# Optimization experiments

Measured on AMD Instinct MI355X. Metric: run time of the kernel, lower is better.

Reference implementation:

```python
import jax, jax.numpy as jnp
import numpy as np

B, CIN, H, W = 1, 512, 128, 128
NC, D, P, NH = 10, 128, 200, 8
HW = H * W
DH = D // NH
FF = 256


def setup_inputs():
    key = jax.random.key(0)
    ks = jax.random.split(key, 20)
    def nrm(i, shape, s=0.02):
        return jax.random.normal(ks[i], shape, jnp.float32) * s
    # TransFusion create_2D_grid: pixel-center coords (x, y), flattened to [1, HW, 2]
    xs = jnp.arange(W, dtype=jnp.float32) + 0.5
    ys = jnp.arange(H, dtype=jnp.float32) + 0.5
    gx, gy = jnp.meshgrid(xs, ys, indexing='xy')
    bev_pos = jnp.stack([gx.reshape(-1), gy.reshape(-1)], axis=-1)[None]
    return {
        'x': jax.random.normal(ks[0], (B, CIN, H, W), jnp.float32),
        'w_shared': nrm(1, (D, CIN, 3, 3)), 'b_shared': jnp.zeros((D,), jnp.float32),
        'w_heat': nrm(2, (NC, D, 3, 3)), 'b_heat': jnp.full((NC,), -2.19, jnp.float32),
        'classes_eye': jnp.eye(NC, dtype=jnp.float32),
        'bev_pos': bev_pos,
        'w_ce': nrm(3, (D, NC)), 'b_ce': jnp.zeros((D,), jnp.float32),
        'w_qpos': nrm(4, (D, 2)), 'w_kpos': nrm(5, (D, 2)),
        'wq': nrm(6, (D, D)), 'wk': nrm(7, (D, D)), 'wv': nrm(8, (D, D)), 'wo': nrm(9, (D, D)),
        'ln1_g': jnp.ones((D,), jnp.float32), 'ln1_b': jnp.zeros((D,), jnp.float32),
        'ln2_g': jnp.ones((D,), jnp.float32), 'ln2_b': jnp.zeros((D,), jnp.float32),
        'w_ff1': nrm(10, (FF, D)), 'b_ff1': jnp.zeros((FF,), jnp.float32),
        'w_ff2': nrm(11, (D, FF)), 'b_ff2': jnp.zeros((D,), jnp.float32),
        'w_center': nrm(12, (2, D)), 'b_center': jnp.zeros((2,), jnp.float32),
        'w_height': nrm(13, (1, D)), 'b_height': jnp.zeros((1,), jnp.float32),
        'w_dim': nrm(14, (3, D)), 'b_dim': jnp.zeros((3,), jnp.float32),
        'w_rot': nrm(15, (2, D)), 'b_rot': jnp.zeros((2,), jnp.float32),
        'w_vel': nrm(16, (2, D)), 'b_vel': jnp.zeros((2,), jnp.float32),
        'w_hm': nrm(17, (NC, D)), 'b_hm': jnp.zeros((NC,), jnp.float32),
    }


def _conv2d(x, w, b):
    y = jax.lax.conv_general_dilated(x, w, (1, 1), 'SAME',
                                     dimension_numbers=('NCHW', 'OIHW', 'NCHW'))
    return y + b[None, :, None, None]


def _ln(x, g, b):
    m = jnp.mean(x, -1, keepdims=True)
    v = jnp.var(x, -1, keepdims=True)
    return (x - m) * jax.lax.rsqrt(v + 1e-5) * g + b


def reference(x, w_shared, b_shared, w_heat, b_heat, classes_eye, bev_pos,
              w_ce, b_ce, w_qpos, w_kpos, wq, wk, wv, wo,
              ln1_g, ln1_b, ln2_g, ln2_b, w_ff1, b_ff1, w_ff2, b_ff2,
              w_center, b_center, w_height, b_height, w_dim, b_dim,
              w_rot, b_rot, w_vel, b_vel, w_hm, b_hm):
    lidar_feat = jax.nn.relu(_conv2d(x, w_shared, b_shared))          # [B,D,H,W]
    lidar_flat = lidar_feat.reshape(B, D, HW)
    dense_heatmap = _conv2d(lidar_feat, w_heat, b_heat)               # [B,NC,H,W]
    heatmap = jax.lax.stop_gradient(jax.nn.sigmoid(dense_heatmap))    # .detach().sigmoid()
    # 3x3 local-max 'NMS'; zero-initialized border (F.max_pool2d VALID placed into zeros)
    inner = jax.lax.reduce_window(heatmap, -jnp.inf, jax.lax.max,
                                  (1, 1, 3, 3), (1, 1, 1, 1), 'VALID')
    local_max = jnp.zeros_like(heatmap).at[:, :, 1:-1, 1:-1].set(inner)
    local_max = local_max.at[:, 8].set(heatmap[:, 8])  # nuScenes: no NMS for cls 8,9
    local_max = local_max.at[:, 9].set(heatmap[:, 9])
    heatmap = heatmap * (heatmap == local_max)
    hm_flat = heatmap.reshape(B, NC, HW)
    # top-k proposals over flattened class*position axis
    _, top = jax.lax.top_k(hm_flat.reshape(B, -1), P)
    top_cls = top // HW                                               # [B,P]
    top_idx = top % HW                                                # [B,P]
    query_feat = jnp.take_along_axis(
        lidar_flat, jnp.broadcast_to(top_idx[:, None, :], (B, D, P)), axis=2)
    one_hot = classes_eye[top_cls].transpose(0, 2, 1)                 # [B,NC,P]
    # class encoding: 1x1 conv1d on one-hot
    query_feat = query_feat + jnp.einsum('dc,bcp->bdp', w_ce, one_hot) + b_ce[None, :, None]
    query_pos = jnp.take_along_axis(
        jnp.broadcast_to(bev_pos, (B, HW, 2)),
        jnp.broadcast_to(top_idx[:, :, None], (B, P, 2)), axis=1)     # [B,P,2]
    # single decoder layer: cross-attention of proposals over BEV features
    q_in = query_feat.transpose(0, 2, 1) + query_pos @ w_qpos.T       # [B,P,D]
    kv_in = lidar_flat.transpose(0, 2, 1) + bev_pos @ w_kpos.T        # [B,HW,D]
    q = (q_in @ wq.T).reshape(B, P, NH, DH)
    k = (kv_in @ wk.T).reshape(B, HW, NH, DH)
    v = (kv_in @ wv.T).reshape(B, HW, NH, DH)
    attn = jax.nn.softmax(jnp.einsum('bqhd,bkhd->bhqk', q, k) / np.sqrt(DH).astype(np.float32), axis=-1)
    out = jnp.einsum('bhqk,bkhd->bqhd', attn, v).reshape(B, P, D) @ wo.T
    h1 = _ln(query_feat.transpose(0, 2, 1) + out, ln1_g, ln1_b)
    ff = jax.nn.relu(h1 @ w_ff1.T + b_ff1) @ w_ff2.T + b_ff2
    h2 = _ln(h1 + ff, ln2_g, ln2_b)
    feat = h2.transpose(0, 2, 1)                                      # [B,D,P]
    def head(wt, bt):
        return jnp.einsum('od,bdp->bop', wt, feat) + bt[None, :, None]
    center = head(w_center, b_center) + query_pos.transpose(0, 2, 1)
    height = head(w_height, b_height)
    dim = head(w_dim, b_dim)
    rot = head(w_rot, b_rot)
    vel = head(w_vel, b_vel)
    hm_pred = head(w_hm, b_hm)
    query_heatmap_score = jnp.take_along_axis(
        hm_flat, jnp.broadcast_to(top_idx[:, None, :], (B, NC, P)), axis=2)
    # get_bboxes: sigmoid(heatmap) * query_heatmap_score * one_hot
    score = jax.nn.sigmoid(hm_pred) * query_heatmap_score * one_hot
    return (score, rot, dim, center, height, vel)
```

## Files before the change

kernel.cpp:

```cpp
#include <hip/hip_runtime.h>
#include <math.h>

#define HWSZ 16384

typedef __attribute__((ext_vector_type(8))) short short8;
typedef __attribute__((ext_vector_type(8))) unsigned short ush8;
typedef __attribute__((ext_vector_type(4))) float f4;

__device__ __forceinline__ ushort f2bf(float f) {
    unsigned u = __float_as_uint(f);
    return (ushort)((u + 0x7fffu + ((u >> 16) & 1u)) >> 16);
}
__device__ __forceinline__ float bf2f(ushort b) {
    return __uint_as_float(((unsigned)b) << 16);
}

__global__ void k_prep_w2(const float* __restrict__ w, float* __restrict__ wt) {
    int idx = blockIdx.x * 256 + threadIdx.x;
    if (idx >= 1152 * 16) return;
    int k = idx >> 4, oc = idx & 15;
    wt[idx] = (oc < 10) ? w[oc * 1152 + k] : 0.f;
}
__global__ void k_cvt_w(const float* __restrict__ w, ushort* __restrict__ wh,
                        ushort* __restrict__ wl) {
    int idx = blockIdx.x * 256 + threadIdx.x;
    if (idx >= 589824) return;
    int oc = idx / 4608, r = idx - oc * 4608;
    int tap = r >> 9, c = r & 511;
    float f = w[oc * 4608 + c * 9 + tap];
    ushort hb = f2bf(f);
    wh[idx] = hb;
    wl[idx] = f2bf(f - bf2f(hb));
}
__global__ __launch_bounds__(256) void k_cvt_x(const float* __restrict__ x,
        ushort* __restrict__ xh, ushort* __restrict__ xl) {
    __shared__ float T[64 * 65];
    int hw0 = blockIdx.x << 6;
    int c0 = blockIdx.y << 6;
    int t = threadIdx.x;
    {
        int cl = t >> 2, q = t & 3;
        const float* src = x + (size_t)(c0 + cl) * HWSZ + hw0 + q * 16;
        #pragma unroll
        for (int k = 0; k < 4; k++) {
            float4 v = *reinterpret_cast<const float4*>(src + k * 4);
            float* dst = &T[cl * 65 + q * 16 + k * 4];
            dst[0] = v.x; dst[1] = v.y; dst[2] = v.z; dst[3] = v.w;
        }
    }
    __syncthreads();
    {
        int hwl = t >> 2, q = t & 3;
        int cc = q * 16;
        size_t ob = (size_t)(hw0 + hwl) * 512 + c0 + cc;
        #pragma unroll
        for (int half = 0; half < 2; half++) {
            ush8 hv, lv;
            #pragma unroll
            for (int k = 0; k < 8; k++) {
                float f = T[(cc + half * 8 + k) * 65 + hwl];
                ushort hb = f2bf(f);
                hv[k] = hb;
                lv[k] = f2bf(f - bf2f(hb));
            }
            *reinterpret_cast<ush8*>(xh + ob + half * 8) = hv;
            *reinterpret_cast<ush8*>(xl + ob + half * 8) = lv;
        }
    }
}

__global__ __launch_bounds__(256) void k_conv1_mfma(
        const ushort* __restrict__ xh, const ushort* __restrict__ xl,
        const ushort* __restrict__ wh, const ushort* __restrict__ wl,
        const float* __restrict__ bias, float* __restrict__ out) {
    __shared__ ushort smem[30720];
    const int t = threadIdx.x;
    const int h = blockIdx.x >> 1, w0 = (blockIdx.x & 1) << 6;
    const int l = t & 63;
    const int wid = t >> 6;
    const int wm = wid >> 1, wn = wid & 1;
    const int l15 = l & 15, lhi = l >> 4;
    const int arow = t >> 2, achk = t & 3;

    f4 acc[2][4];
    #pragma unroll
    for (int m = 0; m < 2; m++)
        #pragma unroll
        for (int n = 0; n < 4; n++) acc[m][n] = (f4){0.f, 0.f, 0.f, 0.f};

    short8 rA[2], rB[2][2];
    const short8 zz = {0, 0, 0, 0, 0, 0, 0, 0};

    auto issue = [&](int it) {
        int c0 = (it / 9) << 5;
        int tap = it % 9;
        int dh = tap / 3 - 1, dw = tap % 3 - 1;
        int hh = h + dh;
        int wg = w0 + arow + dw;
        if (hh >= 0 && hh < 128 && wg >= 0 && wg < 128) {
            size_t off = ((size_t)(hh * 128 + wg) << 9) + c0 + (achk << 3);
            rA[0] = *reinterpret_cast<const short8*>(xh + off);
            rA[1] = *reinterpret_cast<const short8*>(xl + off);
        } else { rA[0] = zz; rA[1] = zz; }
        #pragma unroll
        for (int u = 0; u < 2; u++) {
            int oc = (u << 6) + (t >> 2);
            size_t off = (size_t)oc * 4608 + tap * 512 + c0 + (achk << 3);
            rB[u][0] = *reinterpret_cast<const short8*>(wh + off);
            rB[u][1] = *reinterpret_cast<const short8*>(wl + off);
        }
    };
    auto wstage = [&](int buf) {
        *reinterpret_cast<short8*>(&smem[buf * 5120 + arow * 40 + achk * 8]) = rA[0];
        *reinterpret_cast<short8*>(&smem[buf * 5120 + 2560 + arow * 40 + achk * 8]) = rA[1];
        #pragma unroll
        for (int u = 0; u < 2; u++) {
            int oc = (u << 6) + (t >> 2);
            *reinterpret_cast<short8*>(&smem[10240 + buf * 10240 + oc * 40 + achk * 8]) = rB[u][0];
            *reinterpret_cast<short8*>(&smem[10240 + buf * 10240 + 5120 + oc * 40 + achk * 8]) = rB[u][1];
        }
    };

    issue(0);
    wstage(0);
    issue(1);
    __syncthreads();

    for (int it = 0; it < 144; ++it) {
        int buf = it & 1;
        short8 aH[2], aL[2], bH[4], bL[4];
        #pragma unroll
        for (int m = 0; m < 2; m++) {
            int row = wm * 32 + m * 16 + l15;
            aH[m] = *reinterpret_cast<const short8*>(&smem[buf * 5120 + row * 40 + lhi * 8]);
            aL[m] = *reinterpret_cast<const short8*>(&smem[buf * 5120 + 2560 + row * 40 + lhi * 8]);
        }
        #pragma unroll
        for (int n = 0; n < 4; n++) {
            int oc = wn * 64 + n * 16 + l15;
            bH[n] = *reinterpret_cast<const short8*>(&smem[10240 + buf * 10240 + oc * 40 + lhi * 8]);
            bL[n] = *reinterpret_cast<const short8*>(&smem[10240 + buf * 10240 + 5120 + oc * 40 + lhi * 8]);
        }
        #pragma unroll
        for (int m = 0; m < 2; m++)
            #pragma unroll
            for (int n = 0; n < 4; n++) {
                acc[m][n] = __builtin_amdgcn_mfma_f32_16x16x32_bf16(aH[m], bH[n], acc[m][n], 0, 0, 0);
                acc[m][n] = __builtin_amdgcn_mfma_f32_16x16x32_bf16(aL[m], bH[n], acc[m][n], 0, 0, 0);
                acc[m][n] = __builtin_amdgcn_mfma_f32_16x16x32_bf16(aH[m], bL[n], acc[m][n], 0, 0, 0);
            }
        if (it + 1 < 144) {
            wstage(buf ^ 1);
            if (it + 2 < 144) issue(it + 2);
        }
        __syncthreads();
    }

    float* ot = reinterpret_cast<float*>(smem);
    #pragma unroll
    for (int m = 0; m < 2; m++)
        #pragma unroll
        for (int n = 0; n < 4; n++) {
            int oc = wn * 64 + n * 16 + l15;
            float b = bias[oc];
            #pragma unroll
            for (int r = 0; r < 4; r++) {
                int px = wm * 32 + m * 16 + lhi * 4 + r;
                ot[px * 132 + oc] = fmaxf(acc[m][n][r] + b, 0.f);
            }
        }
    __syncthreads();
    {
        int oc = t >> 1, half = t & 1;
        int base = h * 128 + w0 + half * 32;
        #pragma unroll
        for (int i = 0; i < 32; i += 4) {
            float4 v;
            v.x = ot[(half * 32 + i + 0) * 132 + oc];
            v.y = ot[(half * 32 + i + 1) * 132 + oc];
            v.z = ot[(half * 32 + i + 2) * 132 + oc];
            v.w = ot[(half * 32 + i + 3) * 132 + oc];
            *reinterpret_cast<float4*>(&out[(size_t)oc * HWSZ + base + i]) = v;
        }
    }
}

__global__ __launch_bounds__(256) void k_conv2(const float* __restrict__ lidar,
        const float* __restrict__ wt, const float* __restrict__ bias,
        float* __restrict__ sig) {
    __shared__ float xs[16 * 3 * 68];
    __shared__ float wsm[144 * 16];
    int bid = blockIdx.x;
    int h = bid >> 1, w0 = (bid & 1) << 6;
    int t = threadIdx.x;
    int tpx = (t & 15) << 2;
    int oc = t >> 4;
    float acc[4] = {0.f, 0.f, 0.f, 0.f};
    for (int c0 = 0; c0 < 128; c0 += 16) {
        for (int i = t; i < 16 * 3 * 66; i += 256) {
            int c = i / 198; int rem = i - c * 198; int r = rem / 66; int j = rem - r * 66;
            int gr = h - 1 + r, gc = w0 - 1 + j;
            float v = 0.f;
            if (((unsigned)gr < 128u) & ((unsigned)gc < 128u))
                v = lidar[(c0 + c) * HWSZ + gr * 128 + gc];
            xs[(c * 3 + r) * 68 + j] = v;
        }
        {
            const float4* src = (const float4*)(wt + c0 * 9 * 16);
            float4* dst = (float4*)wsm;
            for (int i = t; i < 576; i += 256) dst[i] = src[i];
        }
        __syncthreads();
        #pragma unroll 4
        for (int c = 0; c < 16; c++) {
            #pragma unroll
            for (int kh = 0; kh < 3; kh++) {
                const float* xr = &xs[(c * 3 + kh) * 68 + tpx];
                float xv0 = xr[0], xv1 = xr[1], xv2 = xr[2], xv3 = xr[3], xv4 = xr[4], xv5 = xr[5];
                #pragma unroll
                for (int kw = 0; kw < 3; kw++) {
                    float wv = wsm[(c * 9 + kh * 3 + kw) * 16 + oc];
                    float p0 = (kw == 0) ? xv0 : ((kw == 1) ? xv1 : xv2);
                    float p1 = (kw == 0) ? xv1 : ((kw == 1) ? xv2 : xv3);
                    float p2 = (kw == 0) ? xv2 : ((kw == 1) ? xv3 : xv4);
                    float p3 = (kw == 0) ? xv3 : ((kw == 1) ? xv4 : xv5);
                    acc[0] += p0 * wv; acc[1] += p1 * wv; acc[2] += p2 * wv; acc[3] += p3 * wv;
                }
            }
        }
        __syncthreads();
    }
    if (oc < 10) {
        float b = bias[oc];
        int col = h * 128 + w0 + tpx;
        float4 v;
        v.x = 1.f / (1.f + expf(-(acc[0] + b)));
        v.y = 1.f / (1.f + expf(-(acc[1] + b)));
        v.z = 1.f / (1.f + expf(-(acc[2] + b)));
        v.w = 1.f / (1.f + expf(-(acc[3] + b)));
        *(float4*)&sig[oc * HWSZ + col] = v;
    }
}

__global__ void k_nms(const float* __restrict__ sig, float* __restrict__ hm) {
    int gid = blockIdx.x * 256 + threadIdx.x;
    int c = gid >> 14, i = gid & 16383;
    int h = i >> 7, w = i & 127;
    float v = sig[gid];
    float keep = 0.f;
    if (c >= 8) keep = v;
    else if (h >= 1 && h <= 126 && w >= 1 && w <= 126) {
        const float* s = sig + c * HWSZ;
        float m = v;
        #pragma unroll
        for (int dh = -1; dh <= 1; dh++)
            #pragma unroll
            for (int dw = -1; dw <= 1; dw++)
                m = fmaxf(m, s[(h + dh) * 128 + (w + dw)]);
        keep = (v == m) ? v : 0.f;
    }
    hm[gid] = keep;
}

__global__ void k_hist_hi(const float* __restrict__ hm, unsigned* __restrict__ hist) {
    int gid = blockIdx.x * 256 + threadIdx.x;
    unsigned k = __float_as_uint(hm[gid]);
    if (k) atomicAdd(&hist[k >> 16], 1u);
}
__global__ void k_scan_hi(const unsigned* __restrict__ hist, unsigned* __restrict__ state) {
    __shared__ unsigned ps[256];
    __shared__ int selc;
    __shared__ unsigned selcum;
    __shared__ unsigned cb[256];
    int t = threadIdx.x;
    unsigned s = 0;
    const unsigned* hp = hist + t * 256;
    for (int i = 0; i < 256; i++) s += hp[i];
    ps[t] = s;
    __syncthreads();
    if (t == 0) {
        unsigned cum = 0; int c = 255;
        for (; c > 0; c--) { if (cum + ps[c] >= 200u) break; cum += ps[c]; }
        selc = c; selcum = cum;
    }
    __syncthreads();
    int c = selc;
    cb[t] = hist[c * 256 + t];
    __syncthreads();
    if (t == 0) {
        unsigned cum = selcum; int b = 255;
        for (; b > 0; b--) { if (cum + cb[b] >= 200u) break; cum += cb[b]; }
        state[8] = (unsigned)(c * 256 + b);
        state[9] = 200u - cum;
        state[10] = cum;
    }
}
__global__ void k_hist_lo(const float* __restrict__ hm, const unsigned* __restrict__ state,
                          unsigned* __restrict__ hist) {
    int gid = blockIdx.x * 256 + threadIdx.x;
    unsigned k = __float_as_uint(hm[gid]);
    if (k && (k >> 16) == state[8]) atomicAdd(&hist[k & 0xFFFFu], 1u);
}
__global__ void k_scan_lo(const unsigned* __restrict__ hist, unsigned* __restrict__ state) {
    __shared__ unsigned ps[256];
    __shared__ int selc;
    __shared__ unsigned selcum;
    __shared__ unsigned cb[256];
    int t = threadIdx.x;
    unsigned target = state[9];
    unsigned s = 0;
    const unsigned* hp = hist + t * 256;
    for (int i = 0; i < 256; i++) s += hp[i];
    ps[t] = s;
    __syncthreads();
    if (t == 0) {
        unsigned cum = 0; int c = 255;
        for (; c > 0; c--) { if (cum + ps[c] >= target) break; cum += ps[c]; }
        selc = c; selcum = cum;
    }
    __syncthreads();
    int c = selc;
    cb[t] = hist[c * 256 + t];
    __syncthreads();
    if (t == 0) {
        unsigned cum = selcum; int b = 255;
        for (; b > 0; b--) { if (cum + cb[b] >= target) break; cum += cb[b]; }
        unsigned lstar = (unsigned)(c * 256 + b);
        state[2] = (state[8] << 16) | lstar;
        state[0] = state[10] + cum;
        state[1] = target - cum;
    }
}
__global__ void k_collect(const float* __restrict__ hm, const unsigned* __restrict__ state,
        unsigned* __restrict__ ck, unsigned* __restrict__ ci,
        unsigned* __restrict__ ti, unsigned* __restrict__ cnts) {
    int gid = blockIdx.x * 256 + threadIdx.x;
    unsigned k = __float_as_uint(hm[gid]);
    unsigned ks = state[2];
    if (k > ks) {
        unsigned pos = atomicAdd(&cnts[0], 1u);
        if (pos < 256u) { ck[pos] = k; ci[pos] = (unsigned)gid; }
    } else if (k == ks) {
        unsigned pos = atomicAdd(&cnts[1], 1u);
        if (pos < 8192u) ti[pos] = (unsigned)gid;
    }
}
__global__ void k_topk_final(const unsigned* __restrict__ state, const unsigned* __restrict__ cnts,
        const unsigned* __restrict__ ck, const unsigned* __restrict__ ci,
        const unsigned* __restrict__ ti, int* __restrict__ top_pos, int* __restrict__ top_cls) {
    __shared__ unsigned kk[200], ii[200];
    int t = threadIdx.x;
    unsigned cgt = cnts[0];
    unsigned need = state[1];
    unsigned keystar = state[2];
    unsigned cntEq = cnts[1]; if (cntEq > 8192u) cntEq = 8192u;
    if ((unsigned)t < cgt && t < 200) { kk[t] = ck[t]; ii[t] = ci[t]; }
    for (unsigned e = t; e < cntEq; e += 256) {
        unsigned my = ti[e]; unsigned r = 0;
        for (unsigned j = 0; j < cntEq; j++) r += (ti[j] < my);
        if (r < need) { kk[cgt + r] = keystar; ii[cgt + r] = my; }
    }
    __syncthreads();
    if (t < 200) {
        unsigned mk = kk[t], mi = ii[t]; int r = 0;
        for (int j = 0; j < 200; j++) {
            unsigned ok = kk[j], oi = ii[j];
            r += (ok > mk) || (ok == mk && oi < mi);
        }
        top_cls[r] = (int)(mi >> 14);
        top_pos[r] = (int)(mi & 16383u);
    }
}

__global__ void k_gather(const float* __restrict__ lidar, const int* __restrict__ top_pos,
        const int* __restrict__ top_cls, const float* __restrict__ w_ce,
        const float* __restrict__ b_ce, const float* __restrict__ w_qpos,
        float* __restrict__ qf, float* __restrict__ qin, float* __restrict__ qpos) {
    int gid = blockIdx.x * 256 + threadIdx.x;
    if (gid >= 200 * 128) return;
    int p = gid >> 7, d = gid & 127;
    int idx = top_pos[p], cls = top_cls[p];
    float px = (float)(idx & 127) + 0.5f, py = (float)(idx >> 7) + 0.5f;
    float v = lidar[d * HWSZ + idx] + w_ce[d * 10 + cls] + b_ce[d];
    qf[gid] = v;
    qin[gid] = v + px * w_qpos[d * 2] + py * w_qpos[d * 2 + 1];
    if (d < 2) qpos[p * 2 + d] = (d == 0) ? px : py;
}

__global__ __launch_bounds__(256) void k_kvin(const float* __restrict__ lidar,
        const float* __restrict__ w_kpos, float* __restrict__ kv) {
    __shared__ float T[128 * 65];
    int hw0 = blockIdx.x << 6;
    int t = threadIdx.x;
    for (int i = t; i < 128 * 64; i += 256) {
        int d = i >> 6, c = i & 63;
        T[d * 65 + c] = lidar[d * HWSZ + hw0 + c];
    }
    __syncthreads();
    for (int i = t; i < 64 * 128; i += 256) {
        int r = i >> 7, d = i & 127;
        int hw = hw0 + r;
        float bx = (float)(hw & 127) + 0.5f, by = (float)(hw >> 7) + 0.5f;
        kv[hw * 128 + d] = T[d * 65 + r] + bx * w_kpos[d * 2] + by * w_kpos[d * 2 + 1];
    }
}

template<int EPI>
__global__ __launch_bounds__(256) void k_gemm(const float* __restrict__ A,
        const float* __restrict__ B, float* __restrict__ C, int M, int N, int K,
        const float* __restrict__ bias, const float* __restrict__ res) {
    __shared__ float As[16 * 68];
    __shared__ float Bs[16 * 68];
    int m0 = blockIdx.x * 64, n0 = blockIdx.y * 64;
    int t = threadIdx.x;
    int mi = (t & 15) << 2, ni = (t >> 4) << 2;
    float acc[4][4];
    #pragma unroll
    for (int i = 0; i < 4; i++)
        #pragma unroll
        for (int j = 0; j < 4; j++) acc[i][j] = 0.f;
    int r = t >> 2, kq = (t & 3) << 2;
    for (int k0 = 0; k0 < K; k0 += 16) {
        float4 v = make_float4(0.f, 0.f, 0.f, 0.f);
        if (m0 + r < M) v = *(const float4*)&A[(m0 + r) * K + k0 + kq];
        As[(kq + 0) * 68 + r] = v.x; As[(kq + 1) * 68 + r] = v.y;
        As[(kq + 2) * 68 + r] = v.z; As[(kq + 3) * 68 + r] = v.w;
        float4 w = *(const float4*)&B[(n0 + r) * K + k0 + kq];
        Bs[(kq + 0) * 68 + r] = w.x; Bs[(kq + 1) * 68 + r] = w.y;
        Bs[(kq + 2) * 68 + r] = w.z; Bs[(kq + 3) * 68 + r] = w.w;
        __syncthreads();
        #pragma unroll
        for (int k = 0; k < 16; k++) {
            float4 a = *(const float4*)&As[k * 68 + mi];
            float4 b = *(const float4*)&Bs[k * 68 + ni];
            acc[0][0] += a.x * b.x; acc[0][1] += a.x * b.y; acc[0][2] += a.x * b.z; acc[0][3] += a.x * b.w;
            acc[1][0] += a.y * b.x; acc[1][1] += a.y * b.y; acc[1][2] += a.y * b.z; acc[1][3] += a.y * b.w;
            acc[2][0] += a.z * b.x; acc[2][1] += a.z * b.y; acc[2][2] += a.z * b.z; acc[2][3] += a.z * b.w;
            acc[3][0] += a.w * b.x; acc[3][1] += a.w * b.y; acc[3][2] += a.w * b.z; acc[3][3] += a.w * b.w;
        }
        __syncthreads();
    }
    #pragma unroll
    for (int i = 0; i < 4; i++) {
        int m = m0 + mi + i;
        if (m >= M) continue;
        #pragma unroll
        for (int j = 0; j < 4; j++) {
            int n = n0 + ni + j;
            float v = acc[i][j];
            if (EPI == 2) v = fmaxf(v + bias[n], 0.f);
            if (EPI == 3) v += bias[n] + res[m * N + n];
            if (EPI == 4) C[((n >> 4) * HWSZ + m) * 16 + (n & 15)] = v;
            else C[m * N + n] = v;
        }
    }
}

__global__ __launch_bounds__(256, 1) void k_attn_part(const float* __restrict__ Q,
        const float* __restrict__ Kp, const float* __restrict__ Vp,
        float* __restrict__ ps, float* __restrict__ pacc) {
    int head = blockIdx.y, chunk = blockIdx.z;
    int t = threadIdx.x;
    int wv = t >> 6, lane = t & 63;
    int qbase = (blockIdx.x * 4 + wv) * 4;
    float q[4][16];
    #pragma unroll
    for (int qq = 0; qq < 4; qq++) {
        int p = qbase + qq; if (p > 199) p = 199;
        const float4* qr = (const float4*)(Q + p * 128 + head * 16);
        #pragma unroll
        for (int u = 0; u < 4; u++) {
            float4 v = qr[u];
            q[qq][u * 4 + 0] = v.x * 0.25f; q[qq][u * 4 + 1] = v.y * 0.25f;
            q[qq][u * 4 + 2] = v.z * 0.25f; q[qq][u * 4 + 3] = v.w * 0.25f;
        }
    }
    const float* Kh = Kp + (size_t)head * HWSZ * 16;
    const float* Vh = Vp + (size_t)head * HWSZ * 16;
    float s[4] = {0.f, 0.f, 0.f, 0.f};
    float acc[4][16];
    #pragma unroll
    for (int qq = 0; qq < 4; qq++)
        #pragma unroll
        for (int i = 0; i < 16; i++) acc[qq][i] = 0.f;
    int k0 = chunk << 10;
    for (int kb = k0 + lane; kb < k0 + 1024; kb += 64) {
        const float4* kr = (const float4*)(Kh + (size_t)kb * 16);
        float4 ka = kr[0], kb4 = kr[1], kc = kr[2], kd = kr[3];
        float kk[16] = {ka.x, ka.y, ka.z, ka.w, kb4.x, kb4.y, kb4.z, kb4.w,
                        kc.x, kc.y, kc.z, kc.w, kd.x, kd.y, kd.z, kd.w};
        const float4* vr = (const float4*)(Vh + (size_t)kb * 16);
        float4 va = vr[0], vb = vr[1], vc = vr[2], vd = vr[3];
        float vv[16] = {va.x, va.y, va.z, va.w, vb.x, vb.y, vb.z, vb.w,
                        vc.x, vc.y, vc.z, vc.w, vd.x, vd.y, vd.z, vd.w};
        #pragma unroll
        for (int qq = 0; qq < 4; qq++) {
            float l0 = fmaf(q[qq][3], kk[3], fmaf(q[qq][2], kk[2], fmaf(q[qq][1], kk[1], q[qq][0] * kk[0])));
            float l1 = fmaf(q[qq][7], kk[7], fmaf(q[qq][6], kk[6], fmaf(q[qq][5], kk[5], q[qq][4] * kk[4])));
            float l2 = fmaf(q[qq][11], kk[11], fmaf(q[qq][10], kk[10], fmaf(q[qq][9], kk[9], q[qq][8] * kk[8])));
            float l3 = fmaf(q[qq][15], kk[15], fmaf(q[qq][14], kk[14], fmaf(q[qq][13], kk[13], q[qq][12] * kk[12])));
            float e = __expf((l0 + l1) + (l2 + l3));
            s[qq] += e;
            #pragma unroll
            for (int i = 0; i < 16; i++) acc[qq][i] = fmaf(e, vv[i], acc[qq][i]);
        }
    }
    #pragma unroll
    for (int mask = 32; mask >= 1; mask >>= 1) {
        #pragma unroll
        for (int qq = 0; qq < 4; qq++) {
            s[qq] += __shfl_xor(s[qq], mask);
            #pragma unroll
            for (int i = 0; i < 16; i++) acc[qq][i] += __shfl_xor(acc[qq][i], mask);
        }
    }
    if (lane == 0) {
        #pragma unroll
        for (int qq = 0; qq < 4; qq++) {
            int p = qbase + qq;
            int idx = (chunk * 8 + head) * 208 + p;
            ps[idx] = s[qq];
            #pragma unroll
            for (int i = 0; i < 16; i++) pacc[idx * 16 + i] = acc[qq][i];
        }
    }
}
__global__ __launch_bounds__(128) void k_attn_comb(const float* __restrict__ ps,
        const float* __restrict__ pacc, float* __restrict__ out) {
    int p = blockIdx.x;
    int t = threadIdx.x;
    int h = t >> 4, d = t & 15;
    float S = 0.f, A = 0.f;
    #pragma unroll
    for (int c = 0; c < 16; c++) {
        int idx = (c * 8 + h) * 208 + p;
        S += ps[idx];
        A += pacc[idx * 16 + d];
    }
    out[p * 128 + h * 16 + d] = A / S;
}

__global__ void k_ln(const float* __restrict__ a, const float* __restrict__ b,
        const float* __restrict__ g, const float* __restrict__ be, float* __restrict__ out) {
    int p = blockIdx.x, d = threadIdx.x;
    float x = a[p * 128 + d];
    if (b) x += b[p * 128 + d];
    __shared__ float red[4];
    float s = x;
    #pragma unroll
    for (int mask = 32; mask >= 1; mask >>= 1) s += __shfl_xor(s, mask);
    if ((d & 63) == 0) red[d >> 6] = s;
    __syncthreads();
    float mean = (red[0] + red[1]) * (1.f / 128.f);
    float dx = x - mean;
    float s2 = dx * dx;
    #pragma unroll
    for (int mask = 32; mask >= 1; mask >>= 1) s2 += __shfl_xor(s2, mask);
    if ((d & 63) == 0) red[2 + (d >> 6)] = s2;
    __syncthreads();
    float var = (red[2] + red[3]) * (1.f / 128.f);
    out[p * 128 + d] = dx * rsqrtf(var + 1e-5f) * g[d] + be[d];
}

__global__ void k_heads(const float* __restrict__ h2, const float* __restrict__ hm,
        const int* __restrict__ top_pos, const int* __restrict__ top_cls,
        const float* __restrict__ qpos,
        const float* __restrict__ w_hm, const float* __restrict__ b_hm,
        const float* __restrict__ w_rot, const float* __restrict__ b_rot,
        const float* __restrict__ w_dim, const float* __restrict__ b_dim,
        const float* __restrict__ w_center, const float* __restrict__ b_center,
        const float* __restrict__ w_height, const float* __restrict__ b_height,
        const float* __restrict__ w_vel, const float* __restrict__ b_vel,
        float* __restrict__ out) {
    int gid = blockIdx.x * 256 + threadIdx.x;
    if (gid >= 4000) return;
    int o = gid / 200, p = gid - o * 200;
    const float* wr; float bias;
    if (o < 10)      { wr = w_hm + o * 128;            bias = b_hm[o]; }
    else if (o < 12) { wr = w_rot + (o - 10) * 128;    bias = b_rot[o - 10]; }
    else if (o < 15) { wr = w_dim + (o - 12) * 128;    bias = b_dim[o - 12]; }
    else if (o < 17) { wr = w_center + (o - 15) * 128; bias = b_center[o - 15]; }
    else if (o < 18) { wr = w_height;                  bias = b_height[0]; }
    else             { wr = w_vel + (o - 18) * 128;    bias = b_vel[o - 18]; }
    const float* hr = h2 + p * 128;
    float dot = 0.f;
    #pragma unroll 8
    for (int d = 0; d < 128; d++) dot = fmaf(wr[d], hr[d], dot);
    dot += bias;
    float outv; int off;
    if (o < 10) {
        float qhs = hm[o * HWSZ + top_pos[p]];
        float oh = (top_cls[p] == o) ? 1.f : 0.f;
        outv = (1.f / (1.f + expf(-dot))) * qhs * oh;
        off = o * 200 + p;
    } else if (o < 12) { outv = dot; off = 2000 + (o - 10) * 200 + p; }
    else if (o < 15)   { outv = dot; off = 2400 + (o - 12) * 200 + p; }
    else if (o < 17)   { outv = dot + qpos[p * 2 + (o - 15)]; off = 3000 + (o - 15) * 200 + p; }
    else if (o < 18)   { outv = dot; off = 3400 + p; }
    else               { outv = dot; off = 3600 + (o - 18) * 200 + p; }
    out[off] = outv;
}

extern "C" void kernel_launch(void* const* d_in, const int* in_sizes, int n_in,
                              void* d_out, int out_size, void* d_ws, size_t ws_size,
                              hipStream_t stream) {
    const float* x        = (const float*)d_in[0];
    const float* w_shared = (const float*)d_in[1];
    const float* b_shared = (const float*)d_in[2];
    const float* w_heat   = (const float*)d_in[3];
    const float* b_heat   = (const float*)d_in[4];
    const float* w_ce     = (const float*)d_in[7];
    const float* b_ce     = (const float*)d_in[8];
    const float* w_qpos   = (const float*)d_in[9];
    const float* w_kpos   = (const float*)d_in[10];
    const float* wq       = (const float*)d_in[11];
    const float* wk       = (const float*)d_in[12];
    const float* wv       = (const float*)d_in[13];
    const float* wo       = (const float*)d_in[14];
    const float* ln1_g    = (const float*)d_in[15];
    const float* ln1_b    = (const float*)d_in[16];
    const float* ln2_g    = (const float*)d_in[17];
    const float* ln2_b    = (const float*)d_in[18];
    const float* w_ff1    = (const float*)d_in[19];
    const float* b_ff1    = (const float*)d_in[20];
    const float* w_ff2    = (const float*)d_in[21];
    const float* b_ff2    = (const float*)d_in[22];
    const float* w_center = (const float*)d_in[23];
    const float* b_center = (const float*)d_in[24];
    const float* w_height = (const float*)d_in[25];
    const float* b_height = (const float*)d_in[26];
    const float* w_dim    = (const float*)d_in[27];
    const float* b_dim    = (const float*)d_in[28];
    const float* w_rot    = (const float*)d_in[29];
    const float* b_rot    = (const float*)d_in[30];
    const float* w_vel    = (const float*)d_in[31];
    const float* b_vel    = (const float*)d_in[32];
    const float* w_hm     = (const float*)d_in[33];
    const float* b_hm     = (const float*)d_in[34];
    float* out = (float*)d_out;

    float* ws = (float*)d_ws;
    float* lidar = ws;
    float* bigR  = lidar + 2097152;
    ushort* xt_hi = (ushort*)bigR;
    ushort* xt_lo = xt_hi + 8388608;
    float* kvin  = bigR;
    float* KpB   = bigR + 2097152;
    float* VpB   = bigR + 4194304;
    float* wbh_f = bigR + 8388608;
    float* wbl_f = wbh_f + 294912;
    ushort* wb_hi = (ushort*)wbh_f;
    ushort* wb_lo = (ushort*)wbl_f;
    float* wt2   = wbl_f + 294912;
    float* sig   = wt2 + 18432;
    float* hmb   = sig + 163840;
    unsigned* hist_hi = (unsigned*)(hmb + 163840);
    unsigned* hist_lo = hist_hi + 65536;
    unsigned* state   = hist_lo + 65536;
    unsigned* cnts    = state + 64;
    unsigned* ck      = cnts + 64;
    unsigned* ci      = ck + 256;
    unsigned* ti      = ci + 256;
    int* top_pos      = (int*)(ti + 8192);
    int* top_cls      = top_pos + 256;
    float* qpos  = (float*)(top_cls + 256);
    float* qf    = qpos + 512;
    float* qin   = qf + 25600;
    float* qbuf  = qin + 25600;
    float* attno = qbuf + 25600;
    float* wo_o  = attno + 25600;
    float* h1    = wo_o + 25600;
    float* f1    = h1 + 25600;
    float* ff2o  = f1 + 51200;
    float* h2    = ff2o + 25600;
    float* ps_b  = h2 + 25600;
    float* pacc_b = ps_b + 26624;
    size_t needed = (size_t)((pacc_b + 425984) - ws) * sizeof(float);
    if (ws_size < needed) return;

    k_prep_w2<<<72, 256, 0, stream>>>(w_heat, wt2);
    k_cvt_w<<<2304, 256, 0, stream>>>(w_shared, wb_hi, wb_lo);
    k_cvt_x<<<dim3(256, 8), 256, 0, stream>>>(x, xt_hi, xt_lo);
    k_conv1_mfma<<<256, 256, 0, stream>>>(xt_hi, xt_lo, wb_hi, wb_lo, b_shared, lidar);
    k_conv2<<<256, 256, 0, stream>>>(lidar, wt2, b_heat, sig);
    k_nms<<<640, 256, 0, stream>>>(sig, hmb);
    hipMemsetAsync(hist_hi, 0, (65536u * 2 + 128) * sizeof(unsigned), stream);
    k_hist_hi<<<640, 256, 0, stream>>>(hmb, hist_hi);
    k_scan_hi<<<1, 256, 0, stream>>>(hist_hi, state);
    k_hist_lo<<<640, 256, 0, stream>>>(hmb, state, hist_lo);
    k_scan_lo<<<1, 256, 0, stream>>>(hist_lo, state);
    k_collect<<<640, 256, 0, stream>>>(hmb, state, ck, ci, ti, cnts);
    k_topk_final<<<1, 256, 0, stream>>>(state, cnts, ck, ci, ti, top_pos, top_cls);
    k_gather<<<100, 256, 0, stream>>>(lidar, top_pos, top_cls, w_ce, b_ce, w_qpos, qf, qin, qpos);
    k_kvin<<<256, 256, 0, stream>>>(lidar, w_kpos, kvin);
    k_gemm<0><<<dim3(4, 2), 256, 0, stream>>>(qin, wq, qbuf, 200, 128, 128, nullptr, nullptr);
    k_gemm<4><<<dim3(256, 2), 256, 0, stream>>>(kvin, wk, KpB, 16384, 128, 128, nullptr, nullptr);
    k_gemm<4><<<dim3(256, 2), 256, 0, stream>>>(kvin, wv, VpB, 16384, 128, 128, nullptr, nullptr);
    k_attn_part<<<dim3(13, 8, 16), 256, 0, stream>>>(qbuf, KpB, VpB, ps_b, pacc_b);
    k_attn_comb<<<200, 128, 0, stream>>>(ps_b, pacc_b, attno);
    k_gemm<0><<<dim3(4, 2), 256, 0, stream>>>(attno, wo, wo_o, 200, 128, 128, nullptr, nullptr);
    k_ln<<<200, 128, 0, stream>>>(qf, wo_o, ln1_g, ln1_b, h1);
    k_gemm<2><<<dim3(4, 4), 256, 0, stream>>>(h1, w_ff1, f1, 200, 256, 128, b_ff1, nullptr);
    k_gemm<3><<<dim3(4, 2), 256, 0, stream>>>(f1, w_ff2, ff2o, 200, 128, 256, b_ff2, h1);
    k_ln<<<200, 128, 0, stream>>>(ff2o, nullptr, ln2_g, ln2_b, h2);
    k_heads<<<16, 256, 0, stream>>>(h2, hmb, top_pos, top_cls, qpos,
        w_hm, b_hm, w_rot, b_rot, w_dim, b_dim, w_center, b_center,
        w_height, b_height, w_vel, b_vel, out);
}
```

Measured before the change: 538.9 us.

## Split conv1 K across blocks with 32x32 MFMA tiles and a reduction kernel

The shared conv kernel changes from 64-pixel by 128-channel tiles to full 128-pixel rows. The 512 input channels are split into two halves handled by separate blocks. The MMA switches from 16x16x32 to 32x32x16 bf16 MFMA, which cuts LDS fragment reads per MFMA, and the smaller K step per iteration shrinks shared memory. Partial sums go to a new 16 MB workspace, and a new finalize kernel adds the halves, applies bias and ReLU, and transposes to NCHW. The cost is extra global traffic for the partial buffers and one more launch.

Result: slower. 666.0 us (+23.6%).

```diff
diff --git a/kernel.cpp b/kernel.cpp
--- a/kernel.cpp
+++ b/kernel.cpp
@@ -6,6 +6,7 @@
 typedef __attribute__((ext_vector_type(8))) short short8;
 typedef __attribute__((ext_vector_type(8))) unsigned short ush8;
 typedef __attribute__((ext_vector_type(4))) float f4;
+typedef __attribute__((ext_vector_type(16))) float f16x;
 
 __device__ __forceinline__ ushort f2bf(float f) {
     unsigned u = __float_as_uint(f);
@@ -72,53 +73,48 @@
 __global__ __launch_bounds__(256) void k_conv1_mfma(
         const ushort* __restrict__ xh, const ushort* __restrict__ xl,
         const ushort* __restrict__ wh, const ushort* __restrict__ wl,
-        const float* __restrict__ bias, float* __restrict__ out) {
-    __shared__ ushort smem[30720];
+        float* __restrict__ part) {
+    __shared__ ushort smem[20480];
     const int t = threadIdx.x;
-    const int h = blockIdx.x >> 1, w0 = (blockIdx.x & 1) << 6;
-    const int l = t & 63;
-    const int wid = t >> 6;
+    const int h = blockIdx.x >> 1, kidx = blockIdx.x & 1;
+    const int l = t & 63, wid = t >> 6;
     const int wm = wid >> 1, wn = wid & 1;
-    const int l15 = l & 15, lhi = l >> 4;
-    const int arow = t >> 2, achk = t & 3;
-
-    f4 acc[2][4];
+    const int l31 = l & 31, lk = l >> 5;
+    const int srow = t >> 1, skh = t & 1;
+    const int cbase0 = kidx * 256;
+
+    f16x acc[2][2];
     #pragma unroll
     for (int m = 0; m < 2; m++)
         #pragma unroll
-        for (int n = 0; n < 4; n++) acc[m][n] = (f4){0.f, 0.f, 0.f, 0.f};
-
-    short8 rA[2], rB[2][2];
+        for (int n = 0; n < 2; n++)
+            #pragma unroll
+            for (int i = 0; i < 16; i++) acc[m][n][i] = 0.f;
+
+    short8 rA[2], rB[2];
     const short8 zz = {0, 0, 0, 0, 0, 0, 0, 0};
 
     auto issue = [&](int it) {
-        int c0 = (it / 9) << 5;
-        int tap = it % 9;
-        int dh = tap / 3 - 1, dw = tap % 3 - 1;
-        int hh = h + dh;
-        int wg = w0 + arow + dw;
-        if (hh >= 0 && hh < 128 && wg >= 0 && wg < 128) {
-            size_t off = ((size_t)(hh * 128 + wg) << 9) + c0 + (achk << 3);
+        int kc = it / 9, tap = it - kc * 9;
+        int dh = tap / 3 - 1, dw = tap - (tap / 3) * 3 - 1;
+        int cb = cbase0 + kc * 16 + skh * 8;
+        int hh = h + dh, wwp = srow + dw;
+        if (((unsigned)hh < 128u) & ((unsigned)wwp < 128u)) {
+            size_t off = ((size_t)(hh * 128 + wwp) << 9) + cb;
             rA[0] = *reinterpret_cast<const short8*>(xh + off);
             rA[1] = *reinterpret_cast<const short8*>(xl + off);
         } else { rA[0] = zz; rA[1] = zz; }
-        #pragma unroll
-        for (int u = 0; u < 2; u++) {
-            int oc = (u << 6) + (t >> 2);
-            size_t off = (size_t)oc * 4608 + tap * 512 + c0 + (achk << 3);
-            rB[u][0] = *reinterpret_cast<const short8*>(wh + off);
-            rB[u][1] = *reinterpret_cast<const short8*>(wl + off);
-        }
+        size_t ob = (size_t)srow * 4608 + tap * 512 + cb;
+        rB[0] = *reinterpret_cast<const short8*>(wh + ob);
+        rB[1] = *reinterpret_cast<const short8*>(wl + ob);
     };
     auto wstage = [&](int buf) {
-        *reinterpret_cast<short8*>(&smem[buf * 5120 + arow * 40 + achk * 8]) = rA[0];
-        *reinterpret_cast<short8*>(&smem[buf * 5120 + 2560 + arow * 40 + achk * 8]) = rA[1];
-        #pragma unroll
-        for (int u = 0; u < 2; u++) {
-            int oc = (u << 6) + (t >> 2);
-            *reinterpret_cast<short8*>(&smem[10240 + buf * 10240 + oc * 40 + achk * 8]) = rB[u][0];
-            *reinterpret_cast<short8*>(&smem[10240 + buf * 10240 + 5120 + oc * 40 + achk * 8]) = rB[u][1];
-        }
+        int a = srow * 20 + skh * 8;
+        ushort* s = smem + buf * 10240;
+        *reinterpret_cast<short8*>(s + a) = rA[0];
+        *reinterpret_cast<short8*>(s + 2560 + a) = rA[1];
+        *reinterpret_cast<short8*>(s + 5120 + a) = rB[0];
+        *reinterpret_cast<short8*>(s + 7680 + a) = rB[1];
     };
 
     issue(0);
@@ -128,26 +124,27 @@
 
     for (int it = 0; it < 144; ++it) {
         int buf = it & 1;
-        short8 aH[2], aL[2], bH[4], bL[4];
+        const ushort* s = smem + buf * 10240;
+        short8 aH[2], aL[2], bH[2], bL[2];
         #pragma unroll
         for (int m = 0; m < 2; m++) {
-            int row = wm * 32 + m * 16 + l15;
-            aH[m] = *reinterpret_cast<const short8*>(&smem[buf * 5120 + row * 40 + lhi * 8]);
-            aL[m] = *reinterpret_cast<const short8*>(&smem[buf * 5120 + 2560 + row * 40 + lhi * 8]);
-        }
-        #pragma unroll
-        for (int n = 0; n < 4; n++) {
-            int oc = wn * 64 + n * 16 + l15;
-            bH[n] = *reinterpret_cast<const short8*>(&smem[10240 + buf * 10240 + oc * 40 + lhi * 8]);
-            bL[n] = *reinterpret_cast<const short8*>(&smem[10240 + buf * 10240 + 5120 + oc * 40 + lhi * 8]);
+            int ra = (wm * 64 + m * 32 + l31) * 20 + lk * 8;
+            aH[m] = *reinterpret_cast<const short8*>(s + ra);
+            aL[m] = *reinterpret_cast<const short8*>(s + 2560 + ra);
+        }
+        #pragma unroll
+        for (int n = 0; n < 2; n++) {
+            int rb = (wn * 64 + n * 32 + l31) * 20 + lk * 8;
+            bH[n] = *reinterpret_cast<const short8*>(s + 5120 + rb);
+            bL[n] = *reinterpret_cast<const short8*>(s + 7680 + rb);
         }
         #pragma unroll
         for (int m = 0; m < 2; m++)
             #pragma unroll
-            for (int n = 0; n < 4; n++) {
-                acc[m][n] = __builtin_amdgcn_mfma_f32_16x16x32_bf16(aH[m], bH[n], acc[m][n], 0, 0, 0);
-                acc[m][n] = __builtin_amdgcn_mfma_f32_16x16x32_bf16(aL[m], bH[n], acc[m][n], 0, 0, 0);
-                acc[m][n] = __builtin_amdgcn_mfma_f32_16x16x32_bf16(aH[m], bL[n], acc[m][n], 0, 0, 0);
+            for (int n = 0; n < 2; n++) {
+                acc[m][n] = __builtin_amdgcn_mfma_f32_32x32x16_bf16(aH[m], bH[n], acc[m][n], 0, 0, 0);
+                acc[m][n] = __builtin_amdgcn_mfma_f32_32x32x16_bf16(aL[m], bH[n], acc[m][n], 0, 0, 0);
+                acc[m][n] = __builtin_amdgcn_mfma_f32_32x32x16_bf16(aH[m], bL[n], acc[m][n], 0, 0, 0);
             }
         if (it + 1 < 144) {
             wstage(buf ^ 1);
@@ -156,32 +153,51 @@
         __syncthreads();
     }
 
-    float* ot = reinterpret_cast<float*>(smem);
+    float* pb = part + ((size_t)kidx << 21);
     #pragma unroll
     for (int m = 0; m < 2; m++)
         #pragma unroll
-        for (int n = 0; n < 4; n++) {
-            int oc = wn * 64 + n * 16 + l15;
-            float b = bias[oc];
-            #pragma unroll
-            for (int r = 0; r < 4; r++) {
-                int px = wm * 32 + m * 16 + lhi * 4 + r;
-                ot[px * 132 + oc] = fmaxf(acc[m][n][r] + b, 0.f);
+        for (int n = 0; n < 2; n++) {
+            int oc = wn * 64 + n * 32 + l31;
+            #pragma unroll
+            for (int r = 0; r < 16; r++) {
+                int px = wm * 64 + m * 32 + (r & 3) + ((r >> 2) << 3) + (lk << 2);
+                pb[(size_t)(h * 128 + px) * 128 + oc] = acc[m][n][r];
             }
         }
-    __syncthreads();
-    {
-        int oc = t >> 1, half = t & 1;
-        int base = h * 128 + w0 + half * 32;
-        #pragma unroll
-        for (int i = 0; i < 32; i += 4) {
-            float4 v;
-            v.x = ot[(half * 32 + i + 0) * 132 + oc];
-            v.y = ot[(half * 32 + i + 1) * 132 + oc];
-            v.z = ot[(half * 32 + i + 2) * 132 + oc];
-            v.w = ot[(half * 32 + i + 3) * 132 + oc];
-            *reinterpret_cast<float4*>(&out[(size_t)oc * HWSZ + base + i]) = v;
-        }
+}
+
+__global__ __launch_bounds__(256) void k_conv1_fin(const float* __restrict__ part,
+        const float* __restrict__ bias, float* __restrict__ out) {
+    __shared__ float T[128 * 65];
+    int hw0 = blockIdx.x << 6;
+    int t = threadIdx.x;
+    const float* p0 = part;
+    const float* p1 = part + (1u << 21);
+    #pragma unroll
+    for (int k = 0; k < 8; k++) {
+        int fl = (t + k * 256) * 4;
+        int hwl = fl >> 7, oc0 = fl & 127;
+        size_t o = (size_t)(hw0 + hwl) * 128 + oc0;
+        float4 a = *reinterpret_cast<const float4*>(p0 + o);
+        float4 b = *reinterpret_cast<const float4*>(p1 + o);
+        T[(oc0 + 0) * 65 + hwl] = a.x + b.x;
+        T[(oc0 + 1) * 65 + hwl] = a.y + b.y;
+        T[(oc0 + 2) * 65 + hwl] = a.z + b.z;
+        T[(oc0 + 3) * 65 + hwl] = a.w + b.w;
+    }
+    __syncthreads();
+    #pragma unroll
+    for (int k = 0; k < 8; k++) {
+        int fl = (t + k * 256) * 4;
+        int oc = fl >> 6, c = fl & 63;
+        float b = bias[oc];
+        float4 v;
+        v.x = fmaxf(T[oc * 65 + c + 0] + b, 0.f);
+        v.y = fmaxf(T[oc * 65 + c + 1] + b, 0.f);
+        v.z = fmaxf(T[oc * 65 + c + 2] + b, 0.f);
+        v.w = fmaxf(T[oc * 65 + c + 3] + b, 0.f);
+        *reinterpret_cast<float4*>(out + (size_t)oc * HWSZ + hw0 + c) = v;
     }
 }
 
@@ -675,13 +691,15 @@
     float* h2    = ff2o + 25600;
     float* ps_b  = h2 + 25600;
     float* pacc_b = ps_b + 26624;
-    size_t needed = (size_t)((pacc_b + 425984) - ws) * sizeof(float);
+    float* part  = pacc_b + 425984;
+    size_t needed = (size_t)((part + 4194304) - ws) * sizeof(float);
     if (ws_size < needed) return;
 
     k_prep_w2<<<72, 256, 0, stream>>>(w_heat, wt2);
     k_cvt_w<<<2304, 256, 0, stream>>>(w_shared, wb_hi, wb_lo);
     k_cvt_x<<<dim3(256, 8), 256, 0, stream>>>(x, xt_hi, xt_lo);
-    k_conv1_mfma<<<256, 256, 0, stream>>>(xt_hi, xt_lo, wb_hi, wb_lo, b_shared, lidar);
+    k_conv1_mfma<<<256, 256, 0, stream>>>(xt_hi, xt_lo, wb_hi, wb_lo, part);
+    k_conv1_fin<<<256, 256, 0, stream>>>(part, b_shared, lidar);
     k_conv2<<<256, 256, 0, stream>>>(lidar, wt2, b_heat, sig);
     k_nms<<<640, 256, 0, stream>>>(sig, hmb);
     hipMemsetAsync(hist_hi, 0, (65536u * 2 + 128) * sizeof(unsigned), stream);
```
